# Performance work log

Measured on AMD Instinct MI355X. Metric: run time of the kernel, lower is better.

The kernel has to match this reference:

```python
import jax, jax.numpy as jnp
import numpy as np
from itertools import combinations

SEQ_LEN = 10; WAY = 5; SHOT = 5; TSS = 2
IN_DIM = 2048; OUT_DIM = 2048
PAIRS = np.array(list(combinations(range(SEQ_LEN), TSS)))  # [T, 2] frame-pair indices
T = PAIRS.shape[0]  # 45 tuples


def _cdist(a, b):
    # Euclidean distance matrix, stable form: sqrt(|a|^2 + |b|^2 - 2 a.b)
    a2 = jnp.sum(a * a, axis=-1)[:, None]
    b2 = jnp.sum(b * b, axis=-1)[None, :]
    sq = a2 + b2 - 2.0 * (a @ b.T)
    return jnp.sqrt(jnp.maximum(sq, 0.0))


def setup_inputs() -> dict:
    key = jax.random.key(0)
    k1, k2, k3, k4 = jax.random.split(key, 4)
    n_s = WAY * SHOT            # 25
    n_q = WAY * 15              # 75
    support_set = jax.random.normal(k1, (n_s, SEQ_LEN, IN_DIM), jnp.float32)
    queries = jax.random.normal(k2, (n_q, SEQ_LEN, IN_DIM), jnp.float32)
    # class-sorted labels: class c occupies rows [c*SHOT, (c+1)*SHOT)
    support_labels = jnp.arange(n_s, dtype=jnp.int32) // SHOT
    lim = 1.0 / np.sqrt(IN_DIM * TSS)
    clsW_w = jax.random.uniform(k3, (OUT_DIM, IN_DIM * TSS), jnp.float32, -lim, lim)
    clsW_b = jax.random.uniform(k4, (OUT_DIM,), jnp.float32, -lim, lim)
    return {"support_set": support_set, "support_labels": support_labels,
            "queries": queries, "clsW_w": clsW_w, "clsW_b": clsW_b}


def _forward(support_set, queries, clsW_w, clsW_b):
    n_s, n_q = support_set.shape[0], queries.shape[0]
    D2 = TSS * IN_DIM
    # tuple gather: [n, T, 2*in_dim] (dropout is eval-mode identity)
    sup = support_set[:, PAIRS, :].reshape(n_s, T, D2)
    qry = queries[:, PAIRS, :].reshape(n_q, T, D2)
    q_embed = jax.nn.relu(qry.reshape(n_q * T, D2) @ clsW_w.T + clsW_b)      # [nqT, D]
    sup_c = sup.reshape(WAY, SHOT * T, D2)                                    # labels sorted by class
    support_all = jax.nn.relu(jnp.einsum('csd,od->cso', sup_c, clsW_w) + clsW_b)  # [way, sT, D]

    distmat = jax.vmap(lambda s: _cdist(q_embed, s))(support_all)             # [way, nqT, sT]
    # torch: view(-1, T, shot).topk(k=1, dim=1).mean -> max over reshaped axis
    dist_class = distmat.reshape(WAY, n_q * T, T, SHOT).max(axis=2)           # [way, nqT, shot]
    ave_dist_all = dist_class.mean(axis=2)                                    # [way, nqT]
    dist_min = distmat.min(axis=2).reshape(WAY, n_q, T).mean(axis=2).T        # [n_q, way] (computed, unused downstream)
    dist_max = distmat.max(axis=2).reshape(WAY, n_q, T).mean(axis=2).T        # [n_q, way]
    pos_all = jnp.argmax(distmat, axis=2)                                     # [way, nqT]

    cols = []
    for c in range(WAY):
        mse = support_all[c][pos_all[c]]                                      # [nqT, D]
        other = support_all[np.array([m for m in range(WAY) if m != c])]      # [way-1, sT, D]
        other_flat = other.reshape((WAY - 1) * SHOT * T, OUT_DIM)
        cosd = _cdist(mse, other_flat).reshape(n_q * T, WAY - 1, SHOT * T)
        cosd = cosd.transpose(1, 0, 2)                                        # [way-1, nqT, sT]
        # record_pos[idx, s2] = #{s1 : cosd[idx,s1,s2] > ave_dist_all[c, s1]}
        record = jnp.sum(cosd > ave_dist_all[c][None, :, None], axis=1).astype(jnp.float32)  # [way-1, sT]
        nz = jnp.maximum(jnp.sum(record != 0, axis=1), 1).astype(jnp.float32)
        thr = record.sum(axis=1) / nz                                         # mean over nonzero entries
        mask = (record < thr[:, None]).astype(jnp.float32)                    # selected columns per other-class
        # diff_embed = concat of selected rows; mean of cdist over them == masked mean
        d_full = _cdist(q_embed, other_flat)                                  # [nqT, (way-1)*sT]
        msum = jnp.maximum(mask.sum(), 1.0)
        mean_d = (d_full * mask.reshape(-1)[None, :]).sum(axis=1) / msum      # [nqT]
        cols.append(mean_d.reshape(n_q, T).mean(axis=1) / (WAY - 1))
    dist_contrast = jnp.stack(cols, axis=1)                                   # [n_q, way]

    logits_contrast = dist_max / (dist_contrast + dist_max)
    return dist_max, logits_contrast


def reference(support_set, support_labels, queries, clsW_w, clsW_b):
    # support_labels are sorted class blocks (arange // shot); class gather is a reshape
    return _forward(support_set, queries, clsW_w, clsW_b)
```

## Files before the change

### kernel.cpp

```cpp
#include <hip/hip_runtime.h>


typedef __bf16 bf16x8 __attribute__((ext_vector_type(8)));
typedef float f32x4 __attribute__((ext_vector_type(4)));

#define NQT   3375
#define MROWS 4500
#define MPAD  4608
#define LDD   1152
#define BK    32

__constant__ int P0[45] = {0,0,0,0,0,0,0,0,0,
                           1,1,1,1,1,1,1,1,
                           2,2,2,2,2,2,2,
                           3,3,3,3,3,3,
                           4,4,4,4,4,
                           5,5,5,5,
                           6,6,6,
                           7,7,
                           8};
__constant__ int P1[45] = {1,2,3,4,5,6,7,8,9,
                           2,3,4,5,6,7,8,9,
                           3,4,5,6,7,8,9,
                           4,5,6,7,8,9,
                           5,6,7,8,9,
                           6,7,8,9,
                           7,8,9,
                           8,9,
                           9};

__device__ inline unsigned short f2b(float x) {
  __bf16 b = (__bf16)x;
  return __builtin_bit_cast(unsigned short, b);
}
__device__ inline float b2f(unsigned int u16) {
  return __uint_as_float(u16 << 16);
}

__device__ __forceinline__ void gl_lds16(const unsigned short* g, unsigned short* l) {
  __builtin_amdgcn_global_load_lds(
      (__attribute__((address_space(1))) void*)(g),
      (__attribute__((address_space(3))) void*)(l),
      16, 0, 0);
}

__global__ void prep(const float* __restrict__ W, const float* __restrict__ Q,
                     const float* __restrict__ Sp,
                     unsigned short* __restrict__ Ws, unsigned short* __restrict__ X,
                     float* __restrict__ record, float* __restrict__ msum) {
  int b = blockIdx.x, tid = threadIdx.x;
  if (b < 8192) {
    int i = b * 256 + tid;
    int i4 = i << 2;
    int o  = i4 >> 12;
    int k  = i4 & 4095;
    int hf = k >> 11;
    int kk = k & 2047;
    float4 v = reinterpret_cast<const float4*>(W)[i];
    ushort4 u;
    u.x = f2b(v.x); u.y = f2b(v.y); u.z = f2b(v.z); u.w = f2b(v.w);
    *reinterpret_cast<ushort4*>(Ws + (size_t)(o + hf * 2048) * 2048 + kk) = u;
  } else if (b < 10240) {
    int i = (b - 8192) * 256 + tid;
    ushort4 u = {0, 0, 0, 0};
    if (i < 384000) {
      float4 v = reinterpret_cast<const float4*>(Q)[i];
      u.x = f2b(v.x); u.y = f2b(v.y); u.z = f2b(v.z); u.w = f2b(v.w);
    } else if (i < 512000) {
      float4 v = reinterpret_cast<const float4*>(Sp)[i - 384000];
      u.x = f2b(v.x); u.y = f2b(v.y); u.z = f2b(v.z); u.w = f2b(v.w);
    }
    reinterpret_cast<ushort4*>(X)[i] = u;
  } else {
    int i = (b - 10240) * 256 + tid;
    if (i < 4500) record[i] = 0.f;
    else if (i < 4505) msum[i - 4500] = 0.f;
  }
}

__global__ __launch_bounds__(256)
void gemm_ring(const unsigned short* __restrict__ A, const unsigned short* __restrict__ B,
               int lda, int ldb, int Ksplit,
               float* __restrict__ Pout0, float* __restrict__ Pout1, int ldd) {
  __shared__ unsigned short As[3][128 * BK];
  __shared__ unsigned short Bs[3][128 * BK];
  const int tid  = threadIdx.x;
  const int wave = tid >> 6, lane = tid & 63;
  const int quad = lane >> 4, l16 = lane & 15;
  const int wm = (wave >> 1) * 64, wn = (wave & 1) * 64;
  const int m0 = blockIdx.x * 128, n0 = blockIdx.y * 128;
  const int kbase = blockIdx.z * Ksplit;

  f32x4 acc[4][4];
#pragma unroll
  for (int i = 0; i < 4; ++i)
#pragma unroll
    for (int j = 0; j < 4; ++j) {
      f32x4 z = {0.f, 0.f, 0.f, 0.f};
      acc[i][j] = z;
    }

  const int r0  = tid >> 2;
  const int qsw = (tid & 3) ^ ((tid >> 3) & 3);
  const int kp0 = qsw * 8;
  const int rsw = (quad ^ ((l16 >> 1) & 3)) * 8;
  const unsigned short* pa0 = A + (size_t)(m0 + r0) * lda + kbase + kp0;
  const unsigned short* pa1 = A + (size_t)(m0 + r0 + 64) * lda + kbase + kp0;
  const unsigned short* pb0 = B + (size_t)(n0 + r0) * ldb + kbase + kp0;
  const unsigned short* pb1 = B + (size_t)(n0 + r0 + 64) * ldb + kbase + kp0;
  const int NKi = Ksplit / BK;

#define ISSUE(kk, st) do {                                   \
    gl_lds16(pa0 + (size_t)(kk) * BK, &As[st][wave * 512]);        \
    gl_lds16(pa1 + (size_t)(kk) * BK, &As[st][2048 + wave * 512]); \
    gl_lds16(pb0 + (size_t)(kk) * BK, &Bs[st][wave * 512]);        \
    gl_lds16(pb1 + (size_t)(kk) * BK, &Bs[st][2048 + wave * 512]); \
  } while (0)

  ISSUE(0, 0);
  ISSUE(1, 1);
  asm volatile("s_waitcnt vmcnt(4)" ::: "memory");
  __builtin_amdgcn_s_barrier();

  int sc = 0;
  for (int k = 0; k < NKi; ++k) {
    int sn = sc + 2; if (sn >= 3) sn -= 3;
    if (k + 2 < NKi) ISSUE(k + 2, sn);
    bf16x8 af[4], bfr[4];
#pragma unroll
    for (int t = 0; t < 4; ++t)
      af[t] = *reinterpret_cast<const bf16x8*>(&As[sc][(wm + t * 16 + l16) * BK + rsw]);
#pragma unroll
    for (int t = 0; t < 4; ++t)
      bfr[t] = *reinterpret_cast<const bf16x8*>(&Bs[sc][(wn + t * 16 + l16) * BK + rsw]);
#pragma unroll
    for (int i = 0; i < 4; ++i)
#pragma unroll
      for (int j = 0; j < 4; ++j)
        acc[i][j] = __builtin_amdgcn_mfma_f32_16x16x32_bf16(af[i], bfr[j], acc[i][j], 0, 0, 0);
    if (k + 1 < NKi) {
      if (k + 2 < NKi) asm volatile("s_waitcnt vmcnt(4)" ::: "memory");
      else             asm volatile("s_waitcnt vmcnt(0)" ::: "memory");
      __builtin_amdgcn_s_barrier();
    }
    sc = sc + 1; if (sc >= 3) sc = 0;
  }
#undef ISSUE
  asm volatile("s_waitcnt vmcnt(0)" ::: "memory");

  float* Pout = blockIdx.z ? Pout1 : Pout0;
#pragma unroll
  for (int i = 0; i < 4; ++i)
#pragma unroll
    for (int j = 0; j < 4; ++j) {
      int col = n0 + wn + j * 16 + l16;
      int rbase = m0 + wm + i * 16 + quad * 4;
      f32x4 v = acc[i][j];
#pragma unroll
      for (int r = 0; r < 4; ++r)
        Pout[(size_t)(rbase + r) * ldd + col] = v[r];
    }
}

__global__ void build_e(const float* __restrict__ Y0, const float* __restrict__ Y1,
                        const float* __restrict__ bias,
                        unsigned short* __restrict__ E, float* __restrict__ sq) {
  int r = blockIdx.x, tid = threadIdx.x;
  if (r >= MROWS) {
    uint4 z = {0, 0, 0, 0};
    reinterpret_cast<uint4*>(E + (size_t)r * 2048)[tid] = z;
    if (tid == 0) sq[r] = 0.f;
    return;
  }
  int x0, x1;
  if (r < NQT) {
    int n = r / 45, t = r - n * 45;
    x0 = n * 10 + P0[t]; x1 = n * 10 + P1[t];
  } else {
    int rr = r - NQT;
    int c = rr / 225, j = rr - c * 225;
    int sh = j / 45, t = j - sh * 45;
    int s = 750 + (c * 5 + sh) * 10;
    x0 = s + P0[t]; x1 = s + P1[t];
  }
  const float4* ya0 = reinterpret_cast<const float4*>(Y0 + (size_t)x0 * 4096) + tid * 2;
  const float4* yb0 = reinterpret_cast<const float4*>(Y1 + (size_t)x0 * 4096) + tid * 2;
  const float4* ya1 = reinterpret_cast<const float4*>(Y0 + (size_t)x1 * 4096 + 2048) + tid * 2;
  const float4* yb1 = reinterpret_cast<const float4*>(Y1 + (size_t)x1 * 4096 + 2048) + tid * 2;
  const float4* bz  = reinterpret_cast<const float4*>(bias) + tid * 2;
  float s = 0.f;
  unsigned short o[8];
#pragma unroll
  for (int h = 0; h < 2; ++h) {
    float4 a = ya0[h], a2 = yb0[h], b = ya1[h], b2 = yb1[h], c = bz[h];
    float v[4] = {a.x + a2.x + b.x + b2.x + c.x,
                  a.y + a2.y + b.y + b2.y + c.y,
                  a.z + a2.z + b.z + b2.z + c.z,
                  a.w + a2.w + b.w + b2.w + c.w};
#pragma unroll
    for (int u = 0; u < 4; ++u) {
      float x = fmaxf(v[u], 0.f);
      unsigned short ob = f2b(x);
      o[h * 4 + u] = ob;
      float xr = b2f(ob);
      s += xr * xr;
    }
  }
  reinterpret_cast<uint4*>(E + (size_t)r * 2048)[tid] = *reinterpret_cast<uint4*>(o);
  __shared__ float red[256];
  red[tid] = s;
  __syncthreads();
  for (int st = 128; st > 0; st >>= 1) {
    if (tid < st) red[tid] += red[tid + st];
    __syncthreads();
  }
  if (tid == 0) sq[r] = red[0];
}

__global__ void dist_fix(const float* __restrict__ Pa, const float* __restrict__ Pb,
                         const float* __restrict__ sq, float* __restrict__ D) {
  int i = blockIdx.x * 256 + threadIdx.x;
  if (i >= MPAD * LDD / 4) return;
  int row = i / (LDD / 4);
  int c0  = (i - row * (LDD / 4)) * 4;
  float4 a = reinterpret_cast<const float4*>(Pa)[i];
  float4 b = reinterpret_cast<const float4*>(Pb)[i];
  float sr = sq[row];
  float4 o;
  o.x = sqrtf(fmaxf(sr + sq[NQT + c0 + 0] - 2.f * (a.x + b.x), 0.f));
  o.y = sqrtf(fmaxf(sr + sq[NQT + c0 + 1] - 2.f * (a.y + b.y), 0.f));
  o.z = sqrtf(fmaxf(sr + sq[NQT + c0 + 2] - 2.f * (a.z + b.z), 0.f));
  o.w = sqrtf(fmaxf(sr + sq[NQT + c0 + 3] - 2.f * (a.w + b.w), 0.f));
  reinterpret_cast<float4*>(D)[i] = o;
}

__global__ __launch_bounds__(256)
void stats_wave(const float* __restrict__ D, float* __restrict__ ave,
                int* __restrict__ pos, float* __restrict__ rmax) {
  __shared__ float sm[4][64];
  int wv = threadIdx.x >> 6, lane = threadIdx.x & 63;
  int i = blockIdx.x * 4 + wv;
  int c = blockIdx.y;
  if (i >= NQT) return;
  const float* p = D + (size_t)i * LDD + c * 225;
  float best = -1e30f; int bi = 225;
  float gm = -1e30f;
  if (lane < 60) {
#pragma unroll
    for (int r = 0; r < 4; ++r) {
      int j = lane + 60 * r;
      if (j < 225) {
        float v = p[j];
        if (v > best) { best = v; bi = j; }
        gm = fmaxf(gm, v);
      }
    }
  }
#pragma unroll
  for (int s = 32; s > 0; s >>= 1) {
    float vv = __shfl_down(best, s, 64);
    int   ii = __shfl_down(bi,   s, 64);
    if (vv > best || (vv == best && ii < bi)) { best = vv; bi = ii; }
  }
  sm[wv][lane] = gm;
  __builtin_amdgcn_wave_barrier();
  if (lane < 5) {
    float m = -1e30f;
#pragma unroll
    for (int a = 0; a < 12; ++a) m = fmaxf(m, sm[wv][lane + 5 * a]);
    sm[wv][lane] = m;
  }
  __builtin_amdgcn_wave_barrier();
  if (lane == 0) {
    float s5 = sm[wv][0] + sm[wv][1] + sm[wv][2] + sm[wv][3] + sm[wv][4];
    ave[c * NQT + i]  = s5 * 0.2f;
    pos[c * NQT + i]  = bi;
    rmax[c * NQT + i] = best;
  }
}

__global__ void record_part(const float* __restrict__ D, const float* __restrict__ ave,
                            const int* __restrict__ pos, float* __restrict__ record) {
  int b = blockIdx.x;
  int c = b / 135, chunk = b - c * 135;
  int i0 = chunk * 25;
  int tid = threadIdx.x;
  __shared__ int   sp[25];
  __shared__ float sa[25];
  if (tid < 25) {
    sp[tid] = pos[c * NQT + i0 + tid];
    sa[tid] = ave[c * NQT + i0 + tid];
  }
  __syncthreads();
  float cnt[4] = {0.f, 0.f, 0.f, 0.f};
  int gcol[4];
#pragma unroll
  for (int j = 0; j < 4; ++j) {
    int col = tid + j * 256;
    gcol[j] = (col < 900) ? (col < c * 225 ? col : col + 225) : 0;
  }
  const bool act3 = (tid + 768) < 900;
  const float* Dsup = D + (size_t)(NQT + c * 225) * LDD;
  for (int ii = 0; ii < 25; ++ii) {
    const float* row = Dsup + (size_t)sp[ii] * LDD;
    float a = sa[ii];
    cnt[0] += (row[gcol[0]] > a) ? 1.f : 0.f;
    cnt[1] += (row[gcol[1]] > a) ? 1.f : 0.f;
    cnt[2] += (row[gcol[2]] > a) ? 1.f : 0.f;
    if (act3) cnt[3] += (row[gcol[3]] > a) ? 1.f : 0.f;
  }
#pragma unroll
  for (int j = 0; j < 4; ++j) {
    int col = tid + j * 256;
    if (col < 900) atomicAdd(&record[c * 900 + col], cnt[j]);
  }
}

__global__ void record_finish(const float* __restrict__ record, float* __restrict__ mask,
                              float* __restrict__ msum) {
  int b = blockIdx.x;
  int c = b / 4, mi = b - c * 4;
  int tid = threadIdx.x;
  float r = (tid < 225) ? record[c * 900 + mi * 225 + tid] : 0.f;
  __shared__ float s1[256], s2[256];
  __shared__ float thr_s;
  s1[tid] = r;
  s2[tid] = (tid < 225 && r != 0.f) ? 1.f : 0.f;
  __syncthreads();
  for (int st = 128; st > 0; st >>= 1) {
    if (tid < st) { s1[tid] += s1[tid + st]; s2[tid] += s2[tid + st]; }
    __syncthreads();
  }
  if (tid == 0) {
    float nz = s2[0] < 1.f ? 1.f : s2[0];
    thr_s = s1[0] / nz;
  }
  __syncthreads();
  float m = 0.f;
  if (tid < 225) {
    m = (r < thr_s) ? 1.f : 0.f;
    mask[(c * 4 + mi) * 225 + tid] = m;
  }
  s1[tid] = m;
  __syncthreads();
  for (int st = 128; st > 0; st >>= 1) {
    if (tid < st) s1[tid] += s1[tid + st];
    __syncthreads();
  }
  if (tid == 0) atomicAdd(&msum[c], s1[0]);
}

__global__ __launch_bounds__(256)
void contrast_rows(const float* __restrict__ D, const float* __restrict__ mask,
                   float* __restrict__ S) {
  int wave = threadIdx.x >> 6, lane = threadIdx.x & 63;
  int i = blockIdx.x * 4 + wave;
  int c = blockIdx.y;
  if (i >= NQT) return;
  const float* row = D + (size_t)i * LDD;
  const float* mk  = mask + c * 900;
  const int cbase = c * 225;
  float acc = 0.f;
#pragma unroll
  for (int k = 0; k < 15; ++k) {
    int col = k * 64 + lane;
    if (col < 900) {
      int gcol = col + (col >= cbase ? 225 : 0);
      acc += mk[col] * row[gcol];
    }
  }
#pragma unroll
  for (int s = 32; s > 0; s >>= 1) acc += __shfl_down(acc, s, 64);
  if (lane == 0) S[c * NQT + i] = acc;
}

__global__ void final_kernel(const float* __restrict__ S, const float* __restrict__ msum,
                             const float* __restrict__ rmax, float* __restrict__ out) {
  int gid = blockIdx.x * 256 + threadIdx.x;
  if (gid >= 375) return;
  int q = gid / 5, c = gid - q * 5;
  float dsum = 0.f, ssum = 0.f;
  for (int t = 0; t < 45; ++t) {
    dsum += rmax[c * NQT + q * 45 + t];
    ssum += S[c * NQT + q * 45 + t];
  }
  float dm = dsum / 45.f;
  float ms = msum[c]; if (ms < 1.f) ms = 1.f;
  float contrast = ssum / (ms * 180.f);
  out[q * 5 + c] = dm;
  out[375 + q * 5 + c] = dm / (contrast + dm);
}

extern "C" void kernel_launch(void* const* d_in, const int* in_sizes, int n_in,
                              void* d_out, int out_size, void* d_ws, size_t ws_size,
                              hipStream_t stream) {
  const float* support = (const float*)d_in[0];
  const float* queries = (const float*)d_in[2];
  const float* W       = (const float*)d_in[3];
  const float* bias    = (const float*)d_in[4];
  float* out = (float*)d_out;

  char* ws = (char*)d_ws;
  size_t off = 0;
  unsigned short* Xb  = (unsigned short*)(ws + off);
  unsigned short* Wsp = (unsigned short*)(ws + off + 4194304);
  float*          Pd1 = (float*)(ws + off);          off += 21233664;
  float*          Y0  = (float*)(ws + off);          off += (size_t)1024 * 4096 * 4;
  float*          Dm  = (float*)(ws + off);
  float*          Y1  = (float*)(ws + off);          off += (size_t)MPAD * LDD * 4;
  unsigned short* Eb  = (unsigned short*)(ws + off); off += (size_t)MPAD * 2048 * 2;
  float* sq      = (float*)(ws + off); off += 4608 * 4 + 256;
  float* ave     = (float*)(ws + off); off += 5 * NQT * 4 + 256;
  int*   pos     = (int*)(ws + off);   off += 5 * NQT * 4 + 256;
  float* rmax    = (float*)(ws + off); off += 5 * NQT * 4 + 256;
  float* mask    = (float*)(ws + off); off += 5 * 4 * 225 * 4 + 256;
  float* record  = (float*)(ws + off); off += 5 * 900 * 4 + 256;
  float* Sbuf    = (float*)(ws + off); off += 5 * NQT * 4 + 256;
  float* msum    = (float*)(ws + off); off += 5 * 4 + 256;

  prep<<<10258, 256, 0, stream>>>(W, queries, support, Wsp, Xb, record, msum);

  dim3 g1(1024 / 128, 4096 / 128, 2);
  gemm_ring<<<g1, 256, 0, stream>>>(Xb, Wsp, 2048, 2048, 1024, Y0, Y1, 4096);

  build_e<<<MPAD, 256, 0, stream>>>(Y0, Y1, bias, Eb, sq);

  dim3 g2(MPAD / 128, LDD / 128, 2);
  gemm_ring<<<g2, 256, 0, stream>>>(Eb, Eb + (size_t)NQT * 2048, 2048, 2048, 1024,
                                    Dm, Pd1, LDD);

  dist_fix<<<(MPAD * LDD / 4 + 255) / 256, 256, 0, stream>>>(Dm, Pd1, sq, Dm);

  dim3 gs((NQT + 3) / 4, 5);
  stats_wave<<<gs, 256, 0, stream>>>(Dm, ave, pos, rmax);
  record_part<<<675, 256, 0, stream>>>(Dm, ave, pos, record);
  record_finish<<<20, 256, 0, stream>>>(record, mask, msum);
  dim3 gc((NQT + 3) / 4, 5);
  contrast_rows<<<gc, 256, 0, stream>>>(Dm, mask, Sbuf);
  final_kernel<<<2, 256, 0, stream>>>(Sbuf, msum, rmax, out);
}
```

Baseline: 232.7 us.

## Build pair embeddings from per-frame sums and fuse distance fixup with row stats

The embedding builder now stages each sample's 10 frame partial sums (left and right halves) in shared memory and forms all 45 pair rows from them. The old version re-read four global rows per tuple row, and the new one accumulates squared norms with wave reductions plus atomics, with sq zeroed in prep. The separate dist_fix and stats_wave kernels are merged into one per-row kernel that computes the distances, writes them, and reduces per-class max/argmax/average from shared memory. This removes a kernel launch and a full re-read of the distance matrix. Padding rows 4500..4607 are no longer written to D, and the E stores become scalar 2-byte writes.

```diff
diff --git a/kernel.cpp b/kernel.cpp
--- a/kernel.cpp
+++ b/kernel.cpp
@@ -47,7 +47,8 @@
 __global__ void prep(const float* __restrict__ W, const float* __restrict__ Q,
                      const float* __restrict__ Sp,
                      unsigned short* __restrict__ Ws, unsigned short* __restrict__ X,
-                     float* __restrict__ record, float* __restrict__ msum) {
+                     float* __restrict__ record, float* __restrict__ msum,
+                     float* __restrict__ sq) {
   int b = blockIdx.x, tid = threadIdx.x;
   if (b < 8192) {
     int i = b * 256 + tid;
@@ -75,6 +76,7 @@
     int i = (b - 10240) * 256 + tid;
     if (i < 4500) record[i] = 0.f;
     else if (i < 4505) msum[i - 4500] = 0.f;
+    else if (i < 4505 + 4608) sq[i - 4505] = 0.f;
   }
 }
 
@@ -162,87 +164,86 @@
     }
 }
 
-__global__ void build_e(const float* __restrict__ Y0, const float* __restrict__ Y1,
-                        const float* __restrict__ bias,
-                        unsigned short* __restrict__ E, float* __restrict__ sq) {
-  int r = blockIdx.x, tid = threadIdx.x;
-  if (r >= MROWS) {
+__global__ __launch_bounds__(256)
+void build_e2(const float* __restrict__ Y0, const float* __restrict__ Y1,
+              const float* __restrict__ bias,
+              unsigned short* __restrict__ E, float* __restrict__ sq) {
+  int b = blockIdx.x, tid = threadIdx.x;
+  if (b >= 400) {
+    const size_t base = (size_t)4500 * 2048 / 8;
+    const int total = 108 * 2048 / 8;
     uint4 z = {0, 0, 0, 0};
-    reinterpret_cast<uint4*>(E + (size_t)r * 2048)[tid] = z;
-    if (tid == 0) sq[r] = 0.f;
+    for (int i = (b - 400) * 256 + tid; i < total; i += 512)
+      reinterpret_cast<uint4*>(E)[base + i] = z;
     return;
   }
-  int x0, x1;
-  if (r < NQT) {
-    int n = r / 45, t = r - n * 45;
-    x0 = n * 10 + P0[t]; x1 = n * 10 + P1[t];
-  } else {
-    int rr = r - NQT;
-    int c = rr / 225, j = rr - c * 225;
-    int sh = j / 45, t = j - sh * 45;
-    int s = 750 + (c * 5 + sh) * 10;
-    x0 = s + P0[t]; x1 = s + P1[t];
-  }
-  const float4* ya0 = reinterpret_cast<const float4*>(Y0 + (size_t)x0 * 4096) + tid * 2;
-  const float4* yb0 = reinterpret_cast<const float4*>(Y1 + (size_t)x0 * 4096) + tid * 2;
-  const float4* ya1 = reinterpret_cast<const float4*>(Y0 + (size_t)x1 * 4096 + 2048) + tid * 2;
-  const float4* yb1 = reinterpret_cast<const float4*>(Y1 + (size_t)x1 * 4096 + 2048) + tid * 2;
-  const float4* bz  = reinterpret_cast<const float4*>(bias) + tid * 2;
-  float s = 0.f;
-  unsigned short o[8];
-#pragma unroll
-  for (int h = 0; h < 2; ++h) {
-    float4 a = ya0[h], a2 = yb0[h], b = ya1[h], b2 = yb1[h], c = bz[h];
-    float v[4] = {a.x + a2.x + b.x + b2.x + c.x,
-                  a.y + a2.y + b.y + b2.y + c.y,
-                  a.z + a2.z + b.z + b2.z + c.z,
-                  a.w + a2.w + b.w + b2.w + c.w};
-#pragma unroll
-    for (int u = 0; u < 4; ++u) {
-      float x = fmaxf(v[u], 0.f);
+  int n = b >> 2, q = b & 3;
+  int c0 = q * 512;
+  __shared__ float Lf[10][512];
+  __shared__ float Rf[10][512];
+  for (int e = tid; e < 1280; e += 256) {
+    int f  = e >> 7;
+    int cc = (e & 127) << 2;
+    const float* ya = Y0 + (size_t)(n * 10 + f) * 4096;
+    const float* yb = Y1 + (size_t)(n * 10 + f) * 4096;
+    float4 l0 = *reinterpret_cast<const float4*>(ya + c0 + cc);
+    float4 l1 = *reinterpret_cast<const float4*>(yb + c0 + cc);
+    float4 r0 = *reinterpret_cast<const float4*>(ya + 2048 + c0 + cc);
+    float4 r1 = *reinterpret_cast<const float4*>(yb + 2048 + c0 + cc);
+    float4 L = {l0.x + l1.x, l0.y + l1.y, l0.z + l1.z, l0.w + l1.w};
+    float4 R = {r0.x + r1.x, r0.y + r1.y, r0.z + r1.z, r0.w + r1.w};
+    *reinterpret_cast<float4*>(&Lf[f][cc]) = L;
+    *reinterpret_cast<float4*>(&Rf[f][cc]) = R;
+  }
+  __syncthreads();
+  int wv = tid >> 6, lane = tid & 63;
+  int erow0 = (n < 75) ? n * 45 : NQT + (n - 75) * 45;
+  for (int t = wv; t < 45; t += 4) {
+    int f0 = P0[t], f1 = P1[t];
+    int row = erow0 + t;
+    float s = 0.f;
+#pragma unroll
+    for (int k = 0; k < 8; ++k) {
+      int c = lane + 64 * k;
+      float x = Lf[f0][c] + Rf[f1][c] + bias[c0 + c];
+      x = fmaxf(x, 0.f);
       unsigned short ob = f2b(x);
-      o[h * 4 + u] = ob;
+      E[(size_t)row * 2048 + c0 + c] = ob;
       float xr = b2f(ob);
       s += xr * xr;
     }
-  }
-  reinterpret_cast<uint4*>(E + (size_t)r * 2048)[tid] = *reinterpret_cast<uint4*>(o);
-  __shared__ float red[256];
-  red[tid] = s;
-  __syncthreads();
-  for (int st = 128; st > 0; st >>= 1) {
-    if (tid < st) red[tid] += red[tid + st];
-    __syncthreads();
-  }
-  if (tid == 0) sq[r] = red[0];
-}
-
-__global__ void dist_fix(const float* __restrict__ Pa, const float* __restrict__ Pb,
-                         const float* __restrict__ sq, float* __restrict__ D) {
-  int i = blockIdx.x * 256 + threadIdx.x;
-  if (i >= MPAD * LDD / 4) return;
-  int row = i / (LDD / 4);
-  int c0  = (i - row * (LDD / 4)) * 4;
-  float4 a = reinterpret_cast<const float4*>(Pa)[i];
-  float4 b = reinterpret_cast<const float4*>(Pb)[i];
+#pragma unroll
+    for (int sh = 32; sh > 0; sh >>= 1) s += __shfl_down(s, sh, 64);
+    if (lane == 0) atomicAdd(&sq[row], s);
+  }
+}
+
+__global__ __launch_bounds__(320)
+void dist_stats(const float* __restrict__ Pa, const float* __restrict__ Pb,
+                const float* __restrict__ sq, float* __restrict__ D,
+                float* __restrict__ ave, int* __restrict__ pos,
+                float* __restrict__ rmax) {
+  __shared__ float drow[LDD];
+  __shared__ float sm[5][64];
+  int row = blockIdx.x, tid = threadIdx.x;
   float sr = sq[row];
-  float4 o;
-  o.x = sqrtf(fmaxf(sr + sq[NQT + c0 + 0] - 2.f * (a.x + b.x), 0.f));
-  o.y = sqrtf(fmaxf(sr + sq[NQT + c0 + 1] - 2.f * (a.y + b.y), 0.f));
-  o.z = sqrtf(fmaxf(sr + sq[NQT + c0 + 2] - 2.f * (a.z + b.z), 0.f));
-  o.w = sqrtf(fmaxf(sr + sq[NQT + c0 + 3] - 2.f * (a.w + b.w), 0.f));
-  reinterpret_cast<float4*>(D)[i] = o;
-}
-
-__global__ __launch_bounds__(256)
-void stats_wave(const float* __restrict__ D, float* __restrict__ ave,
-                int* __restrict__ pos, float* __restrict__ rmax) {
-  __shared__ float sm[4][64];
-  int wv = threadIdx.x >> 6, lane = threadIdx.x & 63;
-  int i = blockIdx.x * 4 + wv;
-  int c = blockIdx.y;
-  if (i >= NQT) return;
-  const float* p = D + (size_t)i * LDD + c * 225;
+  if (tid < 288) {
+    int c = tid * 4;
+    size_t ix = (size_t)row * LDD / 4 + tid;
+    float4 a = reinterpret_cast<const float4*>(Pa)[ix];
+    float4 bb = reinterpret_cast<const float4*>(Pb)[ix];
+    float4 o;
+    o.x = sqrtf(fmaxf(sr + sq[NQT + c + 0] - 2.f * (a.x + bb.x), 0.f));
+    o.y = sqrtf(fmaxf(sr + sq[NQT + c + 1] - 2.f * (a.y + bb.y), 0.f));
+    o.z = sqrtf(fmaxf(sr + sq[NQT + c + 2] - 2.f * (a.z + bb.z), 0.f));
+    o.w = sqrtf(fmaxf(sr + sq[NQT + c + 3] - 2.f * (a.w + bb.w), 0.f));
+    reinterpret_cast<float4*>(D)[ix] = o;
+    *reinterpret_cast<float4*>(&drow[c]) = o;
+  }
+  __syncthreads();
+  if (row >= NQT) return;
+  int wv = tid >> 6, lane = tid & 63;
+  const float* p = &drow[wv * 225];
   float best = -1e30f; int bi = 225;
   float gm = -1e30f;
   if (lane < 60) {
@@ -273,9 +274,9 @@
   __builtin_amdgcn_wave_barrier();
   if (lane == 0) {
     float s5 = sm[wv][0] + sm[wv][1] + sm[wv][2] + sm[wv][3] + sm[wv][4];
-    ave[c * NQT + i]  = s5 * 0.2f;
-    pos[c * NQT + i]  = bi;
-    rmax[c * NQT + i] = best;
+    ave[wv * NQT + row]  = s5 * 0.2f;
+    pos[wv * NQT + row]  = bi;
+    rmax[wv * NQT + row] = best;
   }
 }
 
@@ -418,21 +419,19 @@
   float* Sbuf    = (float*)(ws + off); off += 5 * NQT * 4 + 256;
   float* msum    = (float*)(ws + off); off += 5 * 4 + 256;
 
-  prep<<<10258, 256, 0, stream>>>(W, queries, support, Wsp, Xb, record, msum);
+  prep<<<10276, 256, 0, stream>>>(W, queries, support, Wsp, Xb, record, msum, sq);
 
   dim3 g1(1024 / 128, 4096 / 128, 2);
   gemm_ring<<<g1, 256, 0, stream>>>(Xb, Wsp, 2048, 2048, 1024, Y0, Y1, 4096);
 
-  build_e<<<MPAD, 256, 0, stream>>>(Y0, Y1, bias, Eb, sq);
+  build_e2<<<402, 256, 0, stream>>>(Y0, Y1, bias, Eb, sq);
 
   dim3 g2(MPAD / 128, LDD / 128, 2);
   gemm_ring<<<g2, 256, 0, stream>>>(Eb, Eb + (size_t)NQT * 2048, 2048, 2048, 1024,
                                     Dm, Pd1, LDD);
 
-  dist_fix<<<(MPAD * LDD / 4 + 255) / 256, 256, 0, stream>>>(Dm, Pd1, sq, Dm);
-
-  dim3 gs((NQT + 3) / 4, 5);
-  stats_wave<<<gs, 256, 0, stream>>>(Dm, ave, pos, rmax);
+  dist_stats<<<MROWS, 320, 0, stream>>>(Dm, Pd1, sq, Dm, ave, pos, rmax);
+
   record_part<<<675, 256, 0, stream>>>(Dm, ave, pos, record);
   record_finish<<<20, 256, 0, stream>>>(record, mask, msum);
   dim3 gc((NQT + 3) / 4, 5);
```

Result: faster. 221.5 us, median of 2 (-4.9%).
